# Optimization experiments

Hardware: AMD Instinct MI355X
Metric: run time of the kernel (lower is better)

Reference implementation:

```python
import jax, jax.numpy as jnp
import numpy as np

B = 32768


def _mk(key, shape, scale=0.05):
    return (jax.random.normal(key, shape, dtype=jnp.float32) * scale)


def setup_inputs() -> dict:
    key = jax.random.key(0)
    ks = jax.random.split(key, 24)
    inp = {
        "p_i": jax.random.normal(ks[0], (B, 512), dtype=jnp.float32),
        "speed": jax.random.normal(ks[1], (B,), dtype=jnp.float32),
        "command": jax.random.randint(ks[2], (B,), 0, 4),
        "sp_W1": _mk(ks[3], (1, 128)), "sp_b1": jnp.zeros((128,), jnp.float32),
        "sp_W2": _mk(ks[4], (128, 128)), "sp_b2": jnp.zeros((128,), jnp.float32),
        "sp_W3": _mk(ks[5], (128, 128)), "sp_b3": jnp.zeros((128,), jnp.float32),
        # speed_pred_module: 512 -> 128 -> 128 -> 1
        "vp_W1": _mk(ks[6], (512, 128)), "vp_b1": jnp.zeros((128,), jnp.float32),
        "vp_W2": _mk(ks[7], (128, 128)), "vp_b2": jnp.zeros((128,), jnp.float32),
        "vp_W3": _mk(ks[8], (128, 1)), "vp_b3": jnp.zeros((1,), jnp.float32),
        # join_module: Linear(640, 512)
        "join_W": _mk(ks[9], (640, 512)), "join_b": jnp.zeros((512,), jnp.float32),
        # 4 control heads: 512 -> 256 -> 256 -> 3 (stacked over expert axis e)
        "ctrl_W1": _mk(ks[10], (4, 512, 256)), "ctrl_b1": jnp.zeros((4, 256), jnp.float32),
        "ctrl_W2": _mk(ks[11], (4, 256, 256)), "ctrl_b2": jnp.zeros((4, 256), jnp.float32),
        "ctrl_W3": _mk(ks[12], (4, 256, 3)), "ctrl_b3": jnp.zeros((4, 3), jnp.float32),
    }
    return inp


def _mlp3(x, W1, b1, W2, b2, W3, b3):
    h = jax.nn.relu(x @ W1 + b1)
    h = jax.nn.relu(h @ W2 + b2)
    return h @ W3 + b3


def reference(p_i, speed, command,
              sp_W1, sp_b1, sp_W2, sp_b2, sp_W3, sp_b3,
              vp_W1, vp_b1, vp_W2, vp_b2, vp_W3, vp_b3,
              join_W, join_b,
              ctrl_W1, ctrl_b1, ctrl_W2, ctrl_b2, ctrl_W3, ctrl_b3):
    v = _mlp3(speed[:, None], sp_W1, sp_b1, sp_W2, sp_b2, sp_W3, sp_b3)
    # join: [B, 640] -> [B, 512]
    joined = jnp.concatenate([p_i, v], axis=1) @ join_W + join_b
    # speed prediction [B,1]
    v_p = _mlp3(p_i, vp_W1, vp_b1, vp_W2, vp_b2, vp_W3, vp_b3)
    # command-indexed routing: compute all 4 tiny heads batched, then select.
    h = jax.nn.relu(jnp.einsum('bd,edh->beh', joined, ctrl_W1) + ctrl_b1)  # [B,4,256]
    h = jax.nn.relu(jnp.einsum('beh,ehk->bek', h, ctrl_W2) + ctrl_b2)      # [B,4,256]
    a = jnp.einsum('beh,ehk->bek', h, ctrl_W3) + ctrl_b3                    # [B,4,3]
    action = jnp.take_along_axis(a, command[:, None, None], axis=1)[:, 0, :]  # [B,3]
    return (v_p, action)
```

## Files before the change

### kernel.cpp

```cpp
#include <hip/hip_runtime.h>
#include <stdint.h>

#define NROWS 32768

typedef float f32x4 __attribute__((ext_vector_type(4)));
typedef __bf16 bfx8 __attribute__((ext_vector_type(8)));
typedef unsigned uint4v __attribute__((ext_vector_type(4)));

static __device__ __forceinline__ unsigned short f2bf(float f) {
    unsigned u = __builtin_bit_cast(unsigned, f);
    u += 0x7fffu + ((u >> 16) & 1u);
    return (unsigned short)(u >> 16);
}

static __device__ __forceinline__ uint4v cvt8(f32x4 a, f32x4 b) {
    union { __bf16 h[8]; uint4v u; } p;
#pragma unroll
    for (int i = 0; i < 4; ++i) { p.h[i] = (__bf16)a[i]; p.h[4 + i] = (__bf16)b[i]; }
    return p.u;
}

static __device__ __forceinline__ f32x4 mfma16(bfx8 a, bfx8 b, f32x4 c) {
    return __builtin_amdgcn_mfma_f32_16x16x32_bf16(a, b, c, 0, 0, 0);
}

static __device__ __forceinline__ int swz(int row, int col) {
    return col ^ ((row & 7) << 3);
}

static constexpr size_t JOINED_B = 0;
static constexpr size_t V_B      = 33554432;
static constexpr size_t WCT_B    = 41943040;
static constexpr size_t SPW2T_B  = 42762240;
static constexpr size_t SPW3T_B  = 42795008;
static constexpr size_t VPW2T_B  = 42827776;
static constexpr size_t VPW3T_B  = 42860544;
static constexpr size_t C1T_B    = 42864640;
static constexpr size_t C2T_B    = 43913216;
static constexpr size_t C3T_B    = 44437504;
static constexpr size_t CNT_B    = 44470272;
static constexpr size_t SORTED_B = 44470336;
static constexpr size_t WS_NEED  = 44994624;

__global__ __launch_bounds__(256) void k_prep(
    const float* joinW, const float* vpW1, const float* spW2, const float* spW3,
    const float* vpW2, const float* vpW3, const float* c1, const float* c2, const float* c3,
    unsigned short* wct, unsigned short* spw2t, unsigned short* spw3t,
    unsigned short* vpw2t, unsigned short* vpw3t,
    unsigned short* c1t, unsigned short* c2t, unsigned short* c3t, int* cnt)
{
    int bid = blockIdx.x, tid = threadIdx.x;
    if (bid == 0 && tid < 16) cnt[tid] = 0;
    int region, s0;
    if      (bid < 256)  { region = 0; s0 = bid * 1024; }
    else if (bid < 320)  { region = 1; s0 = (bid - 256) * 1024; }
    else if (bid < 336)  { region = 2; s0 = (bid - 320) * 1024; }
    else if (bid < 352)  { region = 3; s0 = (bid - 336) * 1024; }
    else if (bid < 368)  { region = 4; s0 = (bid - 352) * 1024; }
    else if (bid < 384)  { region = 5; s0 = (bid - 368) * 1024; }
    else if (bid < 386)  { region = 6; s0 = (bid - 384) * 1024; }
    else if (bid < 898)  { region = 7; s0 = (bid - 386) * 1024; }
    else if (bid < 1154) { region = 8; s0 = (bid - 898) * 1024; }
    else                 { region = 9; s0 = (bid - 1154) * 1024; }
    for (int j = 0; j < 4; ++j) {
        int s = s0 + tid + j * 256;
        switch (region) {
        case 0: { int k = s >> 9, n = s & 511; wct[n * 640 + k] = f2bf(joinW[s]); } break;
        case 1: { int k = s >> 7, n = s & 127; wct[(512 + n) * 640 + k] = f2bf(vpW1[s]); } break;
        case 2: { int n = 512 + (s >> 7), k = 512 + (s & 127); wct[n * 640 + k] = 0; } break;
        case 3: { int k = s >> 7, n = s & 127; spw2t[n * 128 + k] = f2bf(spW2[s]); } break;
        case 4: { int k = s >> 7, n = s & 127; spw3t[n * 128 + k] = f2bf(spW3[s]); } break;
        case 5: { int k = s >> 7, n = s & 127; vpw2t[n * 128 + k] = f2bf(vpW2[s]); } break;
        case 6: { vpw3t[s] = (s < 128) ? f2bf(vpW3[s]) : 0; } break;
        case 7: { int e = s >> 17, k = (s >> 8) & 511, n = s & 255;
                  c1t[e * 131072 + n * 512 + k] = f2bf(c1[s]); } break;
        case 8: { int e = s >> 16, k = (s >> 8) & 255, n = s & 255;
                  c2t[e * 65536 + n * 256 + k] = f2bf(c2[s]); } break;
        case 9: { int e = s >> 12, r = s & 4095, n = r >> 8, k = r & 255;
                  c3t[s] = (n < 3) ? f2bf(c3[e * 768 + k * 3 + n]) : 0; } break;
        }
    }
}

__global__ __launch_bounds__(256) void k_sp(
    const float* speed, const float* spW1, const float* spb1,
    const float* spb2, const float* spb3,
    const unsigned short* spw2t, const unsigned short* spw3t,
    const int* command, int* cnt, int* sorted, unsigned short* v)
{
    __shared__ alignas(16) unsigned short h1[128 * 128];
    __shared__ alignas(16) unsigned short h2[128 * 128];
    __shared__ int lcnt[4], lbase[4];
    int bid = blockIdx.x, tid = threadIdx.x;
    int r0 = bid * 128;

    if (tid < 4) lcnt[tid] = 0;
    __syncthreads();
    int cc = 0, lpos = 0;
    if (tid < 128) { cc = command[r0 + tid] & 3; lpos = atomicAdd(&lcnt[cc], 1); }
    __syncthreads();
    if (tid < 4) lbase[tid] = atomicAdd(&cnt[tid], lcnt[tid]);
    __syncthreads();
    if (tid < 128) sorted[cc * NROWS + lbase[cc] + lpos] = r0 + tid;

    for (int j = 0; j < 64; ++j) {
        int idx = tid + j * 256;
        int row = idx >> 7, col = idx & 127;
        float h = speed[r0 + row] * spW1[col] + spb1[col];
        h = h > 0.f ? h : 0.f;
        h1[row * 128 + swz(row, col)] = f2bf(h);
    }
    __syncthreads();

    int wave = tid >> 6, lane = tid & 63, lq = lane >> 4, lr = lane & 15;
    int wr = wave >> 1, wc = wave & 1;
    f32x4 acc[4][4] = {};
#pragma unroll
    for (int ks = 0; ks < 4; ++ks) {
        bfx8 a[4], b[4];
#pragma unroll
        for (int mt = 0; mt < 4; ++mt) {
            int row = wr * 64 + mt * 16 + lr;
            a[mt] = *(const bfx8*)&h1[row * 128 + swz(row, ks * 32 + lq * 8)];
        }
#pragma unroll
        for (int nt = 0; nt < 4; ++nt) {
            int n = wc * 64 + nt * 16 + lr;
            b[nt] = *(const bfx8*)(spw2t + n * 128 + ks * 32 + lq * 8);
        }
#pragma unroll
        for (int mt = 0; mt < 4; ++mt)
#pragma unroll
            for (int nt = 0; nt < 4; ++nt)
                acc[mt][nt] = mfma16(a[mt], b[nt], acc[mt][nt]);
    }
#pragma unroll
    for (int mt = 0; mt < 4; ++mt)
#pragma unroll
        for (int nt = 0; nt < 4; ++nt)
#pragma unroll
            for (int j = 0; j < 4; ++j) {
                int row = wr * 64 + mt * 16 + lq * 4 + j;
                int col = wc * 64 + nt * 16 + lr;
                float x = acc[mt][nt][j] + spb2[col];
                x = x > 0.f ? x : 0.f;
                h2[row * 128 + swz(row, col)] = f2bf(x);
            }
    __syncthreads();
    f32x4 acc2[4][4] = {};
#pragma unroll
    for (int ks = 0; ks < 4; ++ks) {
        bfx8 a[4], b[4];
#pragma unroll
        for (int mt = 0; mt < 4; ++mt) {
            int row = wr * 64 + mt * 16 + lr;
            a[mt] = *(const bfx8*)&h2[row * 128 + swz(row, ks * 32 + lq * 8)];
        }
#pragma unroll
        for (int nt = 0; nt < 4; ++nt) {
            int n = wc * 64 + nt * 16 + lr;
            b[nt] = *(const bfx8*)(spw3t + n * 128 + ks * 32 + lq * 8);
        }
#pragma unroll
        for (int mt = 0; mt < 4; ++mt)
#pragma unroll
            for (int nt = 0; nt < 4; ++nt)
                acc2[mt][nt] = mfma16(a[mt], b[nt], acc2[mt][nt]);
    }
#pragma unroll
    for (int mt = 0; mt < 4; ++mt)
#pragma unroll
        for (int nt = 0; nt < 4; ++nt)
#pragma unroll
            for (int j = 0; j < 4; ++j) {
                int row = wr * 64 + mt * 16 + lq * 4 + j;
                int col = wc * 64 + nt * 16 + lr;
                v[(size_t)(r0 + row) * 128 + col] = f2bf(acc2[mt][nt][j] + spb3[col]);
            }
}

__global__ __launch_bounds__(256) void k_join(
    const float* p_i, const unsigned short* v, const unsigned short* wct,
    const float* joinb, const float* vpb1,
    const unsigned short* vpw2t, const unsigned short* vpw3t,
    const float* vpb2, const float* vpb3,
    unsigned short* joined, float* out_vp)
{
    __shared__ alignas(16) unsigned short stg[16384];
    int d = blockIdx.x;
    int L = (d & 7) * 160 + (d >> 3);
    int m0 = (L / 5) * 128, n0 = (L % 5) * 128;
    int tid = threadIdx.x, wave = tid >> 6, lane = tid & 63, lq = lane >> 4, lr = lane & 15;
    int wr = wave >> 1, wc = wave & 1;

    int r0t = tid >> 3, s0t = tid & 7;
    int ss = s0t ^ (r0t & 7);
    const float* pA = p_i + (size_t)(m0 + r0t) * 512 + s0t * 8;
    const unsigned short* pAv = v + (size_t)(m0 + r0t) * 128 + s0t * 8;
    const unsigned short* pB = wct + (size_t)(n0 + r0t) * 640 + s0t * 8;
    unsigned short* lA = &stg[r0t * 64 + ss * 8];
    unsigned short* lB = &stg[8192 + r0t * 64 + ss * 8];

    f32x4 raf[4][2];
    uint4v rab[4], rb[4];
#pragma unroll
    for (int c2 = 0; c2 < 4; ++c2) {
        raf[c2][0] = *(const f32x4*)(pA + c2 * 16384);
        raf[c2][1] = *(const f32x4*)(pA + c2 * 16384 + 4);
        rb[c2]     = *(const uint4v*)(pB + c2 * 20480);
    }
    f32x4 acc[4][4] = {};
#pragma unroll 1
    for (int kt = 0; kt < 10; ++kt) {
        if (kt < 8) {
#pragma unroll
            for (int c2 = 0; c2 < 4; ++c2)
                *(uint4v*)(lA + c2 * 2048) = cvt8(raf[c2][0], raf[c2][1]);
        } else {
#pragma unroll
            for (int c2 = 0; c2 < 4; ++c2)
                *(uint4v*)(lA + c2 * 2048) = rab[c2];
        }
#pragma unroll
        for (int c2 = 0; c2 < 4; ++c2)
            *(uint4v*)(lB + c2 * 2048) = rb[c2];
        __syncthreads();
        if (kt < 7) {
#pragma unroll
            for (int c2 = 0; c2 < 4; ++c2) {
                raf[c2][0] = *(const f32x4*)(pA + c2 * 16384 + (kt + 1) * 64);
                raf[c2][1] = *(const f32x4*)(pA + c2 * 16384 + (kt + 1) * 64 + 4);
            }
        } else if (kt < 9) {
#pragma unroll
            for (int c2 = 0; c2 < 4; ++c2)
                rab[c2] = *(const uint4v*)(pAv + c2 * 4096 + (kt + 1 - 8) * 64);
        }
        if (kt < 9) {
#pragma unroll
            for (int c2 = 0; c2 < 4; ++c2)
                rb[c2] = *(const uint4v*)(pB + c2 * 20480 + (kt + 1) * 64);
        }
#pragma unroll
        for (int ks = 0; ks < 2; ++ks) {
            bfx8 a[4], b[4];
#pragma unroll
            for (int mt = 0; mt < 4; ++mt) {
                int row = wr * 64 + mt * 16 + lr;
                a[mt] = *(const bfx8*)&stg[row * 64 + ((ks * 32 + lq * 8) ^ ((row & 7) << 3))];
            }
#pragma unroll
            for (int nt = 0; nt < 4; ++nt) {
                int n = wc * 64 + nt * 16 + lr;
                b[nt] = *(const bfx8*)&stg[8192 + n * 64 + ((ks * 32 + lq * 8) ^ ((n & 7) << 3))];
            }
#pragma unroll
            for (int mt = 0; mt < 4; ++mt)
#pragma unroll
                for (int nt = 0; nt < 4; ++nt)
                    acc[mt][nt] = mfma16(a[mt], b[nt], acc[mt][nt]);
        }
        __syncthreads();
    }

    if (n0 < 512) {
#pragma unroll
        for (int mt = 0; mt < 4; ++mt)
#pragma unroll
            for (int nt = 0; nt < 4; ++nt)
#pragma unroll
                for (int j = 0; j < 4; ++j) {
                    int row = m0 + wr * 64 + mt * 16 + lq * 4 + j;
                    int col = n0 + wc * 64 + nt * 16 + lr;
                    joined[(size_t)row * 512 + col] = f2bf(acc[mt][nt][j] + joinb[col]);
                }
        return;
    }

#pragma unroll
    for (int mt = 0; mt < 4; ++mt)
#pragma unroll
        for (int nt = 0; nt < 4; ++nt)
#pragma unroll
            for (int j = 0; j < 4; ++j) {
                int row = wr * 64 + mt * 16 + lq * 4 + j;
                int col = wc * 64 + nt * 16 + lr;
                float x = acc[mt][nt][j] + vpb1[col];
                x = x > 0.f ? x : 0.f;
                stg[row * 128 + swz(row, col)] = f2bf(x);
            }
    __syncthreads();
    f32x4 acc2[4][4] = {};
#pragma unroll
    for (int ks = 0; ks < 4; ++ks) {
        bfx8 a[4], b[4];
#pragma unroll
        for (int mt = 0; mt < 4; ++mt) {
            int row = wr * 64 + mt * 16 + lr;
            a[mt] = *(const bfx8*)&stg[row * 128 + swz(row, ks * 32 + lq * 8)];
        }
#pragma unroll
        for (int nt = 0; nt < 4; ++nt) {
            int n = wc * 64 + nt * 16 + lr;
            b[nt] = *(const bfx8*)(vpw2t + n * 128 + ks * 32 + lq * 8);
        }
#pragma unroll
        for (int mt = 0; mt < 4; ++mt)
#pragma unroll
            for (int nt = 0; nt < 4; ++nt)
                acc2[mt][nt] = mfma16(a[mt], b[nt], acc2[mt][nt]);
    }
    __syncthreads();
#pragma unroll
    for (int mt = 0; mt < 4; ++mt)
#pragma unroll
        for (int nt = 0; nt < 4; ++nt)
#pragma unroll
            for (int j = 0; j < 4; ++j) {
                int row = wr * 64 + mt * 16 + lq * 4 + j;
                int col = wc * 64 + nt * 16 + lr;
                float x = acc2[mt][nt][j] + vpb2[col];
                x = x > 0.f ? x : 0.f;
                stg[row * 128 + swz(row, col)] = f2bf(x);
            }
    __syncthreads();
    f32x4 acc3[2] = {};
#pragma unroll
    for (int ks = 0; ks < 4; ++ks) {
        bfx8 b = *(const bfx8*)(vpw3t + lr * 128 + ks * 32 + lq * 8);
#pragma unroll
        for (int mt = 0; mt < 2; ++mt) {
            int row = wave * 32 + mt * 16 + lr;
            bfx8 a = *(const bfx8*)&stg[row * 128 + swz(row, ks * 32 + lq * 8)];
            acc3[mt] = mfma16(a, b, acc3[mt]);
        }
    }
    if (lr == 0) {
#pragma unroll
        for (int mt = 0; mt < 2; ++mt)
#pragma unroll
            for (int j = 0; j < 4; ++j) {
                int row = wave * 32 + mt * 16 + lq * 4 + j;
                out_vp[m0 + row] = acc3[mt][j] + vpb3[0];
            }
    }
}

__global__ __launch_bounds__(512) void k_ctrl(
    const unsigned short* joined, const unsigned short* c1t, const unsigned short* c2t,
    const unsigned short* c3t, const float* b1, const float* b2, const float* b3,
    const int* cnt, const int* sorted, float* out_act)
{
    __shared__ alignas(16) unsigned short hls[128 * 256];
    __shared__ alignas(16) unsigned short Ast[128 * 64];
    __shared__ alignas(16) unsigned short Bst[256 * 64];
    __shared__ int ridx[128];
    int bid = blockIdx.x;
    int e = bid >> 8, i = bid & 255;
    int n_e = cnt[e];
    if (i * 128 >= n_e) return;
    int tid = threadIdx.x;
    if (tid < 128) {
        int g = i * 128 + tid;
        ridx[tid] = sorted[e * NROWS + (g < n_e ? g : n_e - 1)];
    }
    __syncthreads();
    int wave = tid >> 6, lane = tid & 63, lq = lane >> 4, lr = lane & 15;
    int wm = wave & 1, wn = wave >> 1;
    const unsigned short* W1 = c1t + e * (256 * 512);
    const unsigned short* W2 = c2t + e * (256 * 256);
    const unsigned short* W3 = c3t + e * (16 * 256);

    f32x4 acc[4][4] = {};
#pragma unroll 1
    for (int kt = 0; kt < 8; ++kt) {
#pragma unroll
        for (int it = 0; it < 2; ++it) {
            int idx = it * 512 + tid;
            int row = idx >> 3, slot = idx & 7;
            uint4v v = *(const uint4v*)(joined + (size_t)ridx[row] * 512 + kt * 64 + slot * 8);
            *(uint4v*)&Ast[row * 64 + (slot ^ (row & 7)) * 8] = v;
        }
#pragma unroll
        for (int it = 0; it < 4; ++it) {
            int idx = it * 512 + tid;
            int n = idx >> 3, slot = idx & 7;
            uint4v v = *(const uint4v*)(W1 + (size_t)n * 512 + kt * 64 + slot * 8);
            *(uint4v*)&Bst[n * 64 + (slot ^ (n & 7)) * 8] = v;
        }
        __syncthreads();
#pragma unroll
        for (int ks = 0; ks < 2; ++ks) {
            bfx8 a[4], b[4];
#pragma unroll
            for (int mt = 0; mt < 4; ++mt) {
                int row = wm * 64 + mt * 16 + lr;
                a[mt] = *(const bfx8*)&Ast[row * 64 + ((ks * 32 + lq * 8) ^ ((row & 7) << 3))];
            }
#pragma unroll
            for (int nt = 0; nt < 4; ++nt) {
                int n = wn * 64 + nt * 16 + lr;
                b[nt] = *(const bfx8*)&Bst[n * 64 + ((ks * 32 + lq * 8) ^ ((n & 7) << 3))];
            }
#pragma unroll
            for (int mt = 0; mt < 4; ++mt)
#pragma unroll
                for (int nt = 0; nt < 4; ++nt)
                    acc[mt][nt] = mfma16(a[mt], b[nt], acc[mt][nt]);
        }
        __syncthreads();
    }
#pragma unroll
    for (int mt = 0; mt < 4; ++mt)
#pragma unroll
        for (int nt = 0; nt < 4; ++nt)
#pragma unroll
            for (int j = 0; j < 4; ++j) {
                int row = wm * 64 + mt * 16 + lq * 4 + j;
                int col = wn * 64 + nt * 16 + lr;
                float x = acc[mt][nt][j] + b1[e * 256 + col];
                x = x > 0.f ? x : 0.f;
                hls[row * 256 + swz(row, col)] = f2bf(x);
            }
    __syncthreads();

    f32x4 acc2[4][4] = {};
#pragma unroll 1
    for (int kt = 0; kt < 4; ++kt) {
#pragma unroll
        for (int it = 0; it < 4; ++it) {
            int idx = it * 512 + tid;
            int n = idx >> 3, slot = idx & 7;
            uint4v v = *(const uint4v*)(W2 + (size_t)n * 256 + kt * 64 + slot * 8);
            *(uint4v*)&Bst[n * 64 + (slot ^ (n & 7)) * 8] = v;
        }
        __syncthreads();
#pragma unroll
        for (int ks = 0; ks < 2; ++ks) {
            bfx8 a[4], b[4];
#pragma unroll
            for (int mt = 0; mt < 4; ++mt) {
                int row = wm * 64 + mt * 16 + lr;
                a[mt] = *(const bfx8*)&hls[row * 256 + swz(row, kt * 64 + ks * 32 + lq * 8)];
            }
#pragma unroll
            for (int nt = 0; nt < 4; ++nt) {
                int n = wn * 64 + nt * 16 + lr;
                b[nt] = *(const bfx8*)&Bst[n * 64 + ((ks * 32 + lq * 8) ^ ((n & 7) << 3))];
            }
#pragma unroll
            for (int mt = 0; mt < 4; ++mt)
#pragma unroll
                for (int nt = 0; nt < 4; ++nt)
                    acc2[mt][nt] = mfma16(a[mt], b[nt], acc2[mt][nt]);
        }
        __syncthreads();
    }
#pragma unroll
    for (int mt = 0; mt < 4; ++mt)
#pragma unroll
        for (int nt = 0; nt < 4; ++nt)
#pragma unroll
            for (int j = 0; j < 4; ++j) {
                int row = wm * 64 + mt * 16 + lq * 4 + j;
                int col = wn * 64 + nt * 16 + lr;
                float x = acc2[mt][nt][j] + b2[e * 256 + col];
                x = x > 0.f ? x : 0.f;
                hls[row * 256 + swz(row, col)] = f2bf(x);
            }
    __syncthreads();

    {
        f32x4 acc3 = {};
#pragma unroll
        for (int ks = 0; ks < 8; ++ks) {
            int row = wave * 16 + lr;
            bfx8 a = *(const bfx8*)&hls[row * 256 + swz(row, ks * 32 + lq * 8)];
            bfx8 b = *(const bfx8*)(W3 + lr * 256 + ks * 32 + lq * 8);
            acc3 = mfma16(a, b, acc3);
        }
#pragma unroll
        for (int j = 0; j < 4; ++j) {
            int row = wave * 16 + lq * 4 + j;
            int g = i * 128 + row;
            if (lr < 3 && g < n_e)
                out_act[(size_t)ridx[row] * 3 + lr] = acc3[j] + b3[e * 3 + lr];
        }
    }
}

extern "C" void kernel_launch(void* const* d_in, const int* in_sizes, int n_in,
                              void* d_out, int out_size, void* d_ws, size_t ws_size,
                              hipStream_t stream) {
    (void)in_sizes; (void)n_in; (void)out_size;
    if (ws_size < WS_NEED) return;

    const float* p_i    = (const float*)d_in[0];
    const float* speed  = (const float*)d_in[1];
    const int*   command= (const int*)d_in[2];
    const float* sp_W1  = (const float*)d_in[3];
    const float* sp_b1  = (const float*)d_in[4];
    const float* sp_W2  = (const float*)d_in[5];
    const float* sp_b2  = (const float*)d_in[6];
    const float* sp_W3  = (const float*)d_in[7];
    const float* sp_b3  = (const float*)d_in[8];
    const float* vp_W1  = (const float*)d_in[9];
    const float* vp_b1  = (const float*)d_in[10];
    const float* vp_W2  = (const float*)d_in[11];
    const float* vp_b2  = (const float*)d_in[12];
    const float* vp_W3  = (const float*)d_in[13];
    const float* vp_b3  = (const float*)d_in[14];
    const float* join_W = (const float*)d_in[15];
    const float* join_b = (const float*)d_in[16];
    const float* ctrl_W1= (const float*)d_in[17];
    const float* ctrl_b1= (const float*)d_in[18];
    const float* ctrl_W2= (const float*)d_in[19];
    const float* ctrl_b2= (const float*)d_in[20];
    const float* ctrl_W3= (const float*)d_in[21];
    const float* ctrl_b3= (const float*)d_in[22];

    char* ws = (char*)d_ws;
    unsigned short* joined = (unsigned short*)(ws + JOINED_B);
    unsigned short* vbuf   = (unsigned short*)(ws + V_B);
    unsigned short* wct    = (unsigned short*)(ws + WCT_B);
    unsigned short* spw2t  = (unsigned short*)(ws + SPW2T_B);
    unsigned short* spw3t  = (unsigned short*)(ws + SPW3T_B);
    unsigned short* vpw2t  = (unsigned short*)(ws + VPW2T_B);
    unsigned short* vpw3t  = (unsigned short*)(ws + VPW3T_B);
    unsigned short* c1t    = (unsigned short*)(ws + C1T_B);
    unsigned short* c2t    = (unsigned short*)(ws + C2T_B);
    unsigned short* c3t    = (unsigned short*)(ws + C3T_B);
    int* cnt    = (int*)(ws + CNT_B);
    int* sorted = (int*)(ws + SORTED_B);

    float* out_vp  = (float*)d_out;
    float* out_act = out_vp + NROWS;

    k_prep<<<1170, 256, 0, stream>>>(join_W, vp_W1, sp_W2, sp_W3, vp_W2, vp_W3,
                                     ctrl_W1, ctrl_W2, ctrl_W3,
                                     wct, spw2t, spw3t, vpw2t, vpw3t, c1t, c2t, c3t, cnt);
    k_sp<<<256, 256, 0, stream>>>(speed, sp_W1, sp_b1, sp_b2, sp_b3,
                                  spw2t, spw3t, command, cnt, sorted, vbuf);
    k_join<<<1280, 256, 0, stream>>>(p_i, vbuf, wct, join_b, vp_b1,
                                     vpw2t, vpw3t, vp_b2, vp_b3, joined, out_vp);
    k_ctrl<<<1024, 512, 0, stream>>>(joined, c1t, c2t, c3t, ctrl_b1, ctrl_b2, ctrl_b3,
                                     cnt, sorted, out_act);
}
```

Before: 278.0 us.

## Pre-convert p_i to bf16 in prep and use direct global-to-LDS loads in ctrl

The prep kernel gains 4096 extra blocks that convert the fp32 p_i activations to a bf16 workspace copy. The join GEMM then streams bf16 A tiles instead of loading fp32 and converting inside the K loop, which halves its A-side reads across the five N-tile blocks that reuse each row. The control kernel replaces register-staged global→LDS copies with global_load_lds intrinsics, using a source-side swizzle to keep the same LDS layout. The cost is an extra full pass over p_i (a 64 MB read and 32 MB write) plus a larger workspace.

```diff
diff --git a/kernel.cpp b/kernel.cpp
--- a/kernel.cpp
+++ b/kernel.cpp
@@ -13,55 +13,69 @@
     return (unsigned short)(u >> 16);
 }
 
-static __device__ __forceinline__ uint4v cvt8(f32x4 a, f32x4 b) {
-    union { __bf16 h[8]; uint4v u; } p;
-#pragma unroll
-    for (int i = 0; i < 4; ++i) { p.h[i] = (__bf16)a[i]; p.h[4 + i] = (__bf16)b[i]; }
-    return p.u;
-}
-
 static __device__ __forceinline__ f32x4 mfma16(bfx8 a, bfx8 b, f32x4 c) {
     return __builtin_amdgcn_mfma_f32_16x16x32_bf16(a, b, c, 0, 0, 0);
 }
 
+static __device__ __forceinline__ void gload_lds16(const void* g, void* l) {
+    __builtin_amdgcn_global_load_lds(
+        (const __attribute__((address_space(1))) void*)g,
+        (__attribute__((address_space(3))) void*)l, 16, 0, 0);
+}
+
 static __device__ __forceinline__ int swz(int row, int col) {
     return col ^ ((row & 7) << 3);
 }
 
 static constexpr size_t JOINED_B = 0;
-static constexpr size_t V_B      = 33554432;
-static constexpr size_t WCT_B    = 41943040;
-static constexpr size_t SPW2T_B  = 42762240;
-static constexpr size_t SPW3T_B  = 42795008;
-static constexpr size_t VPW2T_B  = 42827776;
-static constexpr size_t VPW3T_B  = 42860544;
-static constexpr size_t C1T_B    = 42864640;
-static constexpr size_t C2T_B    = 43913216;
-static constexpr size_t C3T_B    = 44437504;
-static constexpr size_t CNT_B    = 44470272;
-static constexpr size_t SORTED_B = 44470336;
-static constexpr size_t WS_NEED  = 44994624;
+static constexpr size_t PI_B     = 33554432;
+static constexpr size_t V_B      = 67108864;
+static constexpr size_t WCT_B    = 75497472;
+static constexpr size_t SPW2T_B  = 76316672;
+static constexpr size_t SPW3T_B  = 76349440;
+static constexpr size_t VPW2T_B  = 76382208;
+static constexpr size_t VPW3T_B  = 76414976;
+static constexpr size_t C1T_B    = 76419072;
+static constexpr size_t C2T_B    = 77467648;
+static constexpr size_t C3T_B    = 77991936;
+static constexpr size_t CNT_B    = 78024704;
+static constexpr size_t SORTED_B = 78024768;
+static constexpr size_t WS_NEED  = 78549056;
 
 __global__ __launch_bounds__(256) void k_prep(
-    const float* joinW, const float* vpW1, const float* spW2, const float* spW3,
-    const float* vpW2, const float* vpW3, const float* c1, const float* c2, const float* c3,
-    unsigned short* wct, unsigned short* spw2t, unsigned short* spw3t,
+    const float* p_i, const float* joinW, const float* vpW1, const float* spW2,
+    const float* spW3, const float* vpW2, const float* vpW3,
+    const float* c1, const float* c2, const float* c3,
+    unsigned short* pib, unsigned short* wct, unsigned short* spw2t, unsigned short* spw3t,
     unsigned short* vpw2t, unsigned short* vpw3t,
     unsigned short* c1t, unsigned short* c2t, unsigned short* c3t, int* cnt)
 {
     int bid = blockIdx.x, tid = threadIdx.x;
     if (bid == 0 && tid < 16) cnt[tid] = 0;
+    if (bid < 4096) {
+        size_t c0 = (size_t)bid * 1024;
+#pragma unroll
+        for (int j = 0; j < 4; ++j) {
+            size_t c = c0 + tid + j * 256;
+            f32x4 x = *(const f32x4*)(p_i + c * 4);
+            ushort4 o;
+            o.x = f2bf(x[0]); o.y = f2bf(x[1]); o.z = f2bf(x[2]); o.w = f2bf(x[3]);
+            *(ushort4*)(pib + c * 4) = o;
+        }
+        return;
+    }
+    int b = bid - 4096;
     int region, s0;
-    if      (bid < 256)  { region = 0; s0 = bid * 1024; }
-    else if (bid < 320)  { region = 1; s0 = (bid - 256) * 1024; }
-    else if (bid < 336)  { region = 2; s0 = (bid - 320) * 1024; }
-    else if (bid < 352)  { region = 3; s0 = (bid - 336) * 1024; }
-    else if (bid < 368)  { region = 4; s0 = (bid - 352) * 1024; }
-    else if (bid < 384)  { region = 5; s0 = (bid - 368) * 1024; }
-    else if (bid < 386)  { region = 6; s0 = (bid - 384) * 1024; }
-    else if (bid < 898)  { region = 7; s0 = (bid - 386) * 1024; }
-    else if (bid < 1154) { region = 8; s0 = (bid - 898) * 1024; }
-    else                 { region = 9; s0 = (bid - 1154) * 1024; }
+    if      (b < 256)  { region = 0; s0 = b * 1024; }
+    else if (b < 320)  { region = 1; s0 = (b - 256) * 1024; }
+    else if (b < 336)  { region = 2; s0 = (b - 320) * 1024; }
+    else if (b < 352)  { region = 3; s0 = (b - 336) * 1024; }
+    else if (b < 368)  { region = 4; s0 = (b - 352) * 1024; }
+    else if (b < 384)  { region = 5; s0 = (b - 368) * 1024; }
+    else if (b < 386)  { region = 6; s0 = (b - 384) * 1024; }
+    else if (b < 898)  { region = 7; s0 = (b - 386) * 1024; }
+    else if (b < 1154) { region = 8; s0 = (b - 898) * 1024; }
+    else               { region = 9; s0 = (b - 1154) * 1024; }
     for (int j = 0; j < 4; ++j) {
         int s = s0 + tid + j * 256;
         switch (region) {
@@ -180,7 +194,7 @@
 }
 
 __global__ __launch_bounds__(256) void k_join(
-    const float* p_i, const unsigned short* v, const unsigned short* wct,
+    const unsigned short* pib, const unsigned short* v, const unsigned short* wct,
     const float* joinb, const float* vpb1,
     const unsigned short* vpw2t, const unsigned short* vpw3t,
     const float* vpb2, const float* vpb3,
@@ -195,48 +209,37 @@
 
     int r0t = tid >> 3, s0t = tid & 7;
     int ss = s0t ^ (r0t & 7);
-    const float* pA = p_i + (size_t)(m0 + r0t) * 512 + s0t * 8;
+    const unsigned short* pA = pib + (size_t)(m0 + r0t) * 512 + s0t * 8;
     const unsigned short* pAv = v + (size_t)(m0 + r0t) * 128 + s0t * 8;
     const unsigned short* pB = wct + (size_t)(n0 + r0t) * 640 + s0t * 8;
     unsigned short* lA = &stg[r0t * 64 + ss * 8];
     unsigned short* lB = &stg[8192 + r0t * 64 + ss * 8];
 
-    f32x4 raf[4][2];
-    uint4v rab[4], rb[4];
+    uint4v ra[4], rb[4];
 #pragma unroll
     for (int c2 = 0; c2 < 4; ++c2) {
-        raf[c2][0] = *(const f32x4*)(pA + c2 * 16384);
-        raf[c2][1] = *(const f32x4*)(pA + c2 * 16384 + 4);
-        rb[c2]     = *(const uint4v*)(pB + c2 * 20480);
+        ra[c2] = *(const uint4v*)(pA + c2 * 16384);
+        rb[c2] = *(const uint4v*)(pB + c2 * 20480);
     }
     f32x4 acc[4][4] = {};
 #pragma unroll 1
     for (int kt = 0; kt < 10; ++kt) {
-        if (kt < 8) {
-#pragma unroll
-            for (int c2 = 0; c2 < 4; ++c2)
-                *(uint4v*)(lA + c2 * 2048) = cvt8(raf[c2][0], raf[c2][1]);
-        } else {
-#pragma unroll
-            for (int c2 = 0; c2 < 4; ++c2)
-                *(uint4v*)(lA + c2 * 2048) = rab[c2];
-        }
-#pragma unroll
-        for (int c2 = 0; c2 < 4; ++c2)
+#pragma unroll
+        for (int c2 = 0; c2 < 4; ++c2) {
+            *(uint4v*)(lA + c2 * 2048) = ra[c2];
             *(uint4v*)(lB + c2 * 2048) = rb[c2];
+        }
         __syncthreads();
-        if (kt < 7) {
-#pragma unroll
-            for (int c2 = 0; c2 < 4; ++c2) {
-                raf[c2][0] = *(const f32x4*)(pA + c2 * 16384 + (kt + 1) * 64);
-                raf[c2][1] = *(const f32x4*)(pA + c2 * 16384 + (kt + 1) * 64 + 4);
-            }
-        } else if (kt < 9) {
-#pragma unroll
-            for (int c2 = 0; c2 < 4; ++c2)
-                rab[c2] = *(const uint4v*)(pAv + c2 * 4096 + (kt + 1 - 8) * 64);
-        }
         if (kt < 9) {
+            if (kt < 7) {
+#pragma unroll
+                for (int c2 = 0; c2 < 4; ++c2)
+                    ra[c2] = *(const uint4v*)(pA + c2 * 16384 + (kt + 1) * 64);
+            } else {
+#pragma unroll
+                for (int c2 = 0; c2 < 4; ++c2)
+                    ra[c2] = *(const uint4v*)(pAv + c2 * 4096 + (kt + 1 - 8) * 64);
+            }
 #pragma unroll
             for (int c2 = 0; c2 < 4; ++c2)
                 rb[c2] = *(const uint4v*)(pB + c2 * 20480 + (kt + 1) * 64);
@@ -376,17 +379,17 @@
     for (int kt = 0; kt < 8; ++kt) {
 #pragma unroll
         for (int it = 0; it < 2; ++it) {
-            int idx = it * 512 + tid;
-            int row = idx >> 3, slot = idx & 7;
-            uint4v v = *(const uint4v*)(joined + (size_t)ridx[row] * 512 + kt * 64 + slot * 8);
-            *(uint4v*)&Ast[row * 64 + (slot ^ (row & 7)) * 8] = v;
+            int chunk = it * 512 + tid;
+            int row = chunk >> 3, sl = (chunk & 7) ^ (row & 7);
+            gload_lds16(joined + (size_t)ridx[row] * 512 + kt * 64 + sl * 8,
+                        &Ast[(it * 512 + wave * 64) * 8]);
         }
 #pragma unroll
         for (int it = 0; it < 4; ++it) {
-            int idx = it * 512 + tid;
-            int n = idx >> 3, slot = idx & 7;
-            uint4v v = *(const uint4v*)(W1 + (size_t)n * 512 + kt * 64 + slot * 8);
-            *(uint4v*)&Bst[n * 64 + (slot ^ (n & 7)) * 8] = v;
+            int chunk = it * 512 + tid;
+            int n = chunk >> 3, sl = (chunk & 7) ^ (n & 7);
+            gload_lds16(W1 + (size_t)n * 512 + kt * 64 + sl * 8,
+                        &Bst[(it * 512 + wave * 64) * 8]);
         }
         __syncthreads();
 #pragma unroll
@@ -429,10 +432,10 @@
     for (int kt = 0; kt < 4; ++kt) {
 #pragma unroll
         for (int it = 0; it < 4; ++it) {
-            int idx = it * 512 + tid;
-            int n = idx >> 3, slot = idx & 7;
-            uint4v v = *(const uint4v*)(W2 + (size_t)n * 256 + kt * 64 + slot * 8);
-            *(uint4v*)&Bst[n * 64 + (slot ^ (n & 7)) * 8] = v;
+            int chunk = it * 512 + tid;
+            int n = chunk >> 3, sl = (chunk & 7) ^ (n & 7);
+            gload_lds16(W2 + (size_t)n * 256 + kt * 64 + sl * 8,
+                        &Bst[(it * 512 + wave * 64) * 8]);
         }
         __syncthreads();
 #pragma unroll
@@ -521,6 +524,7 @@
 
     char* ws = (char*)d_ws;
     unsigned short* joined = (unsigned short*)(ws + JOINED_B);
+    unsigned short* pib    = (unsigned short*)(ws + PI_B);
     unsigned short* vbuf   = (unsigned short*)(ws + V_B);
     unsigned short* wct    = (unsigned short*)(ws + WCT_B);
     unsigned short* spw2t  = (unsigned short*)(ws + SPW2T_B);
@@ -536,12 +540,13 @@
     float* out_vp  = (float*)d_out;
     float* out_act = out_vp + NROWS;
 
-    k_prep<<<1170, 256, 0, stream>>>(join_W, vp_W1, sp_W2, sp_W3, vp_W2, vp_W3,
+    k_prep<<<5266, 256, 0, stream>>>(p_i, join_W, vp_W1, sp_W2, sp_W3, vp_W2, vp_W3,
                                      ctrl_W1, ctrl_W2, ctrl_W3,
-                                     wct, spw2t, spw3t, vpw2t, vpw3t, c1t, c2t, c3t, cnt);
+                                     pib, wct, spw2t, spw3t, vpw2t, vpw3t,
+                                     c1t, c2t, c3t, cnt);
     k_sp<<<256, 256, 0, stream>>>(speed, sp_W1, sp_b1, sp_b2, sp_b3,
                                   spw2t, spw3t, command, cnt, sorted, vbuf);
-    k_join<<<1280, 256, 0, stream>>>(p_i, vbuf, wct, join_b, vp_b1,
+    k_join<<<1280, 256, 0, stream>>>(pib, vbuf, wct, join_b, vp_b1,
                                      vpw2t, vpw3t, vp_b2, vp_b3, joined, out_vp);
     k_ctrl<<<1024, 512, 0, stream>>>(joined, c1t, c2t, c3t, ctrl_b1, ctrl_b2, ctrl_b3,
                                      cnt, sorted, out_act);
```

Result: no change. 274.2 us (-1.4%).
